# Kernel tuning notes

Measured on AMD Instinct MI355X. Metric: run time of the kernel, lower is better.

Reference implementation:

```python
import jax, jax.numpy as jnp
import numpy as np

EPS = 1e-6
CHUNK = 128  # chunk size for the causal linear-attention scan


def elu_plus_one(x):
    return jax.nn.elu(x) + 1.0


def causal_linear_attention(q, k, v):
    # out_t = (sq_t @ cumsum_{j<=t} sk_j v_j^T) / (sq_t . cumsum_{j<=t} sk_j), clamped
    B, S, D = q.shape
    sq = elu_plus_one(q)
    sk = elu_plus_one(k)
    N = S // CHUNK
    # [N, B, C, D] chunked layout for scan over chunks
    sq_c = sq.reshape(B, N, CHUNK, D).transpose(1, 0, 2, 3)
    sk_c = sk.reshape(B, N, CHUNK, D).transpose(1, 0, 2, 3)
    v_c = v.reshape(B, N, CHUNK, D).transpose(1, 0, 2, 3)
    mask = jnp.tril(jnp.ones((CHUNK, CHUNK), dtype=q.dtype))  # inclusive causal

    def step(carry, inp):
        S_kv, z = carry  # [B,D,D], [B,D] running sums from previous chunks
        sqi, ski, vi = inp
        A = jnp.einsum('bid,bjd->bij', sqi, ski) * mask  # intra-chunk causal scores
        num = jnp.einsum('bij,bje->bie', A, vi) + jnp.einsum('bid,bde->bie', sqi, S_kv)
        den = A.sum(-1) + jnp.einsum('bid,bd->bi', sqi, z)
        out = num / jnp.clip(den, EPS, None)[..., None]
        S_kv = S_kv + jnp.einsum('bcd,bce->bde', ski, vi)
        z = z + ski.sum(axis=1)
        return (S_kv, z), out

    init = (jnp.zeros((B, D, D), q.dtype), jnp.zeros((B, D), q.dtype))
    _, outs = jax.lax.scan(step, init, (sq_c, sk_c, v_c))
    return outs.transpose(1, 0, 2, 3).reshape(B, S, D)


def setup_inputs() -> dict:
    key = jax.random.key(0)
    ks = jax.random.split(key, 8)
    B, S, D = 2, 2048, 1024
    scale = 1.0 / np.sqrt(D)  # realistic init scale for the D x D projections
    return {
        'hidden_states': jax.random.normal(ks[0], (B, S, D), jnp.float32),
        'w_q': jax.random.normal(ks[1], (D, D), jnp.float32) * scale,
        'w_k': jax.random.normal(ks[2], (D, D), jnp.float32) * scale,
        'w_v': jax.random.normal(ks[3], (D, D), jnp.float32) * scale,
        'w_o': jax.random.normal(ks[4], (D, D), jnp.float32) * scale,
        'gate': jnp.zeros((1,), jnp.float32),
        'memory': jax.random.uniform(ks[5], (D, D), jnp.float32) * 0.01,
        'memory_norm': jax.random.uniform(ks[6], (D,), jnp.float32),
    }


def reference(hidden_states, w_q, w_k, w_v, w_o, gate, memory, memory_norm):
    # Projections (torch Linear: x @ W^T)
    q = hidden_states @ w_q.T
    k = hidden_states @ w_k.T
    v = hidden_states @ w_v.T

    # Retrieve from compressive memory (single bank)
    sigma_q = elu_plus_one(q)
    a_mem = sigma_q @ memory
    norm = jnp.clip(sigma_q @ memory_norm, EPS, None)[..., None]
    active = (memory_norm.sum() >= EPS).astype(q.dtype)
    memory_output = active * (a_mem / norm)

    local_output = causal_linear_attention(q, k, v)

    g = jax.nn.sigmoid(gate)  # [1], broadcasts
    output = g * memory_output + (1.0 - g) * local_output
    return output @ w_o.T
```

## Files before the change

kernel.cpp:

```cpp
#include <hip/hip_runtime.h>
#include <cstddef>

#define EPSF 1e-6f

constexpr int D   = 1024;
constexpr int Bv  = 2;
constexpr int S   = 2048;
constexpr int M   = Bv * S;
constexpr int CH  = 256;
constexpr int NCH = S / CH;

constexpr int TSZ  = 128 * 32;
constexpr int TA64 = 64 * 32;

typedef __attribute__((ext_vector_type(8))) short short8;
typedef __attribute__((ext_vector_type(4))) float floatx4;

__device__ __forceinline__ float elu1(float x) { return x > 0.f ? x + 1.f : __expf(x); }
__device__ __forceinline__ float sigmoidf_(float x) { return 1.f / (1.f + __expf(-x)); }
__device__ __forceinline__ unsigned short f2bf(float x) {
    unsigned u = __float_as_uint(x);
    return (unsigned short)((u + 0x7fffu + ((u >> 16) & 1u)) >> 16);
}
__device__ __forceinline__ float bf2f(unsigned short h) {
    return __uint_as_float(((unsigned)h) << 16);
}
__device__ __forceinline__ float wave_reduce(float x) {
#pragma unroll
    for (int off = 32; off > 0; off >>= 1) x += __shfl_down(x, off);
    return x;
}

__device__ __forceinline__ void gl_lds16(const unsigned short* g, unsigned short* l) {
    __builtin_amdgcn_global_load_lds(
        (const __attribute__((address_space(1))) void*)g,
        (__attribute__((address_space(3))) void*)l, 16, 0, 0);
}

__device__ __forceinline__ void gemm256_8ph(const unsigned short* __restrict__ Ag,
                                            const unsigned short* __restrict__ Bg,
                                            unsigned short* sm, int tid,
                                            floatx4 acc[8][4]) {
    const int lane = tid & 63, w = tid >> 6;
    const int wr = w >> 2, wc = w & 3;
    const int fr = lane & 15, gq = lane >> 4;
    const int swz = fr & 7;

    const int r0 = tid >> 3;
    const int c0 = (tid & 7) ^ (r0 & 7);
    const int r1 = (tid + 512) >> 3;
    const int c1 = ((tid + 512) & 7) ^ (r1 & 7);
    const size_t so0 = (size_t)r0 * D + (size_t)c0 * 8;
    const size_t so1 = (size_t)r1 * D + (size_t)c1 * 8;
    unsigned short* const dst0 = sm + tid * 8;
    unsigned short* const dst1 = sm + (tid + 512) * 8;

    auto STG = [&](int kt, int b, int which) {
        const unsigned short* Gs = ((which) < 2 ? Ag : Bg)
            + (size_t)(((which) & 1) * 128) * D + (size_t)(kt) * 64;
        const int slot = (((b) << 2) + (which)) << 13;
        gl_lds16(Gs + so0, dst0 + slot);
        gl_lds16(Gs + so1, dst1 + slot);
    };

    STG(0, 0, 0); STG(0, 0, 1); STG(0, 0, 2); STG(0, 0, 3);
    STG(1, 1, 2); STG(1, 1, 3);
    asm volatile("s_waitcnt vmcnt(4)" ::: "memory");
    __builtin_amdgcn_s_barrier();

    const int NT = D / 64;
    for (int u = 0; u < NT; ++u) {
        const int bu = u & 1;
        const unsigned short* Ah = sm + (((bu << 2) + wr) << 13);
        const unsigned short* Bh = sm + (((bu << 2) + 2 + (wc >> 1)) << 13);
        const int brow = (wc & 1) * 64;
        short8 bfr[4][2];
#pragma unroll
        for (int s = 0; s < 4; ++s) {
            short8 afr[2][2];
#pragma unroll
            for (int i2 = 0; i2 < 2; ++i2)
#pragma unroll
                for (int ks = 0; ks < 2; ++ks)
                    afr[i2][ks] = *(const short8*)&Ah[((s * 2 + i2) * 16 + fr) * 64
                                                      + ((((ks << 2) + gq) ^ swz) << 3)];
            if (s == 0) {
#pragma unroll
                for (int j = 0; j < 4; ++j)
#pragma unroll
                    for (int ks = 0; ks < 2; ++ks)
                        bfr[j][ks] = *(const short8*)&Bh[(brow + j * 16 + fr) * 64
                                                         + ((((ks << 2) + gq) ^ swz) << 3)];
            }
            if (s == 0)      { if (u + 1 < NT) STG(u + 1, bu ^ 1, 0); }
            else if (s == 1) { if (u + 1 < NT) STG(u + 1, bu ^ 1, 1); }
            else if (s == 2) { if (u + 2 < NT) STG(u + 2, bu, 2); }
            else {
                if (u + 2 < NT) {
                    STG(u + 2, bu, 3);
                    asm volatile("s_waitcnt vmcnt(4)" ::: "memory");
                } else if (u + 1 < NT) {
                    asm volatile("s_waitcnt vmcnt(0)" ::: "memory");
                }
            }
            __builtin_amdgcn_s_barrier();
            __builtin_amdgcn_s_setprio(1);
#pragma unroll
            for (int i2 = 0; i2 < 2; ++i2)
#pragma unroll
                for (int j = 0; j < 4; ++j)
#pragma unroll
                    for (int ks = 0; ks < 2; ++ks)
                        acc[s * 2 + i2][j] = __builtin_amdgcn_mfma_f32_16x16x32_bf16(
                            afr[i2][ks], bfr[j][ks], acc[s * 2 + i2][j], 0, 0, 0);
            __builtin_amdgcn_s_setprio(0);
            __builtin_amdgcn_s_barrier();
        }
    }
}

__device__ __forceinline__ void stage128x32(const unsigned short* g, int stride,
                                            unsigned short* lds, int wave, int lane) {
    const int t   = (wave << 6) + lane;
    const int row = t >> 2;
    const int cb  = (((t & 3) ^ ((row >> 1) & 3)) << 3);
    unsigned short* l0 = lds + (wave << 9);
    gl_lds16(g + (size_t)row * stride + cb, l0);
    gl_lds16(g + (size_t)(row + 64) * stride + cb, l0 + 2048);
}

__device__ __forceinline__ void stage64x32(const unsigned short* g, int stride,
                                           unsigned short* lds, int wave, int lane) {
    const int t   = (wave << 6) + lane;
    const int row = t >> 2;
    const int cb  = (((t & 3) ^ ((row >> 1) & 3)) << 3);
    gl_lds16(g + (size_t)row * stride + cb, lds + (wave << 9));
}

__device__ __forceinline__ void mfma_step(const unsigned short* As, const unsigned short* Bs,
                                          int wm, int wn, int fr, int g, floatx4 acc[4][4]) {
    const int off = ((g ^ ((fr >> 1) & 3)) << 3);
    short8 af[4], bf[4];
#pragma unroll
    for (int i = 0; i < 4; ++i) af[i] = *(const short8*)&As[(wm + i * 16 + fr) * 32 + off];
#pragma unroll
    for (int j = 0; j < 4; ++j) bf[j] = *(const short8*)&Bs[(wn + j * 16 + fr) * 32 + off];
#pragma unroll
    for (int i = 0; i < 4; ++i)
#pragma unroll
        for (int j = 0; j < 4; ++j)
            acc[i][j] = __builtin_amdgcn_mfma_f32_16x16x32_bf16(af[i], bf[j], acc[i][j], 0, 0, 0);
}

__device__ __forceinline__ void mfma_step64d(const unsigned short* As, const unsigned short* Bs,
                                             int wm, int wn, int fr, int g,
                                             floatx4 acc[2][4], floatx4 accd[2], short8 bones) {
    const int off = ((g ^ ((fr >> 1) & 3)) << 3);
    short8 af[2], bf[4];
#pragma unroll
    for (int i = 0; i < 2; ++i) af[i] = *(const short8*)&As[(wm + i * 16 + fr) * 32 + off];
#pragma unroll
    for (int j = 0; j < 4; ++j) bf[j] = *(const short8*)&Bs[(wn + j * 16 + fr) * 32 + off];
#pragma unroll
    for (int i = 0; i < 2; ++i) {
#pragma unroll
        for (int j = 0; j < 4; ++j)
            acc[i][j] = __builtin_amdgcn_mfma_f32_16x16x32_bf16(af[i], bf[j], acc[i][j], 0, 0, 0);
        accd[i] = __builtin_amdgcn_mfma_f32_16x16x32_bf16(af[i], bones, accd[i], 0, 0, 0);
    }
}

__device__ __forceinline__ void mfma_step64(const unsigned short* As, const unsigned short* Bs,
                                            int wm, int wn, int fr, int g, floatx4 acc[2][4]) {
    const int off = ((g ^ ((fr >> 1) & 3)) << 3);
    short8 af[2], bf[4];
#pragma unroll
    for (int i = 0; i < 2; ++i) af[i] = *(const short8*)&As[(wm + i * 16 + fr) * 32 + off];
#pragma unroll
    for (int j = 0; j < 4; ++j) bf[j] = *(const short8*)&Bs[(wn + j * 16 + fr) * 32 + off];
#pragma unroll
    for (int i = 0; i < 2; ++i)
#pragma unroll
        for (int j = 0; j < 4; ++j)
            acc[i][j] = __builtin_amdgcn_mfma_f32_16x16x32_bf16(af[i], bf[j], acc[i][j], 0, 0, 0);
}

__device__ __forceinline__ void gemm_loop_db(const unsigned short* Ag, int strideA,
                                             const unsigned short* Bg, int strideB, int Kk,
                                             unsigned short* As, unsigned short* Bs,
                                             int wave, int lane, int wm, int wn, int fr, int g,
                                             floatx4 acc[4][4]) {
    __syncthreads();
    stage128x32(Ag, strideA, As, wave, lane);
    stage128x32(Bg, strideB, Bs, wave, lane);
    int buf = 0;
    for (int k0 = 32; k0 < Kk; k0 += 32) {
        __syncthreads();
        const int nb = buf ^ 1;
        stage128x32(Ag + k0, strideA, As + nb * TSZ, wave, lane);
        stage128x32(Bg + k0, strideB, Bs + nb * TSZ, wave, lane);
        mfma_step(As + buf * TSZ, Bs + buf * TSZ, wm, wn, fr, g, acc);
        buf = nb;
    }
    __syncthreads();
    mfma_step(As + buf * TSZ, Bs + buf * TSZ, wm, wn, fr, g, acc);
}

__device__ __forceinline__ void gemm_loop_db64d(const unsigned short* Ag, int strideA,
                                                const unsigned short* Bg, int strideB, int Kk,
                                                unsigned short* As, unsigned short* Bs,
                                                int wave, int lane, int wm, int wn, int fr, int g,
                                                floatx4 acc[2][4], floatx4 accd[2], short8 bones) {
    __syncthreads();
    stage64x32(Ag, strideA, As, wave, lane);
    stage128x32(Bg, strideB, Bs, wave, lane);
    int buf = 0;
    for (int k0 = 32; k0 < Kk; k0 += 32) {
        __syncthreads();
        const int nb = buf ^ 1;
        stage64x32(Ag + k0, strideA, As + nb * TA64, wave, lane);
        stage128x32(Bg + k0, strideB, Bs + nb * TSZ, wave, lane);
        mfma_step64d(As + buf * TA64, Bs + buf * TSZ, wm, wn, fr, g, acc, accd, bones);
        buf = nb;
    }
    __syncthreads();
    mfma_step64d(As + buf * TA64, Bs + buf * TSZ, wm, wn, fr, g, acc, accd, bones);
}

__device__ __forceinline__ void gemm_loop_db64(const unsigned short* Ag, int strideA,
                                               const unsigned short* Bg, int strideB, int Kk,
                                               unsigned short* As, unsigned short* Bs,
                                               int wave, int lane, int wm, int wn, int fr, int g,
                                               floatx4 acc[2][4]) {
    __syncthreads();
    stage64x32(Ag, strideA, As, wave, lane);
    stage128x32(Bg, strideB, Bs, wave, lane);
    int buf = 0;
    for (int k0 = 32; k0 < Kk; k0 += 32) {
        __syncthreads();
        const int nb = buf ^ 1;
        stage64x32(Ag + k0, strideA, As + nb * TA64, wave, lane);
        stage128x32(Bg + k0, strideB, Bs + nb * TSZ, wave, lane);
        mfma_step64(As + buf * TA64, Bs + buf * TSZ, wm, wn, fr, g, acc);
        buf = nb;
    }
    __syncthreads();
    mfma_step64(As + buf * TA64, Bs + buf * TSZ, wm, wn, fr, g, acc);
}

__global__ __launch_bounds__(256) void prep(const float* __restrict__ h,
                                            const float* __restrict__ w_q, const float* __restrict__ w_k,
                                            const float* __restrict__ w_v, const float* __restrict__ w_o,
                                            const float* __restrict__ memory,
                                            unsigned short* __restrict__ h_b,
                                            unsigned short* __restrict__ wq_b, unsigned short* __restrict__ wk_b,
                                            unsigned short* __restrict__ wv_b, unsigned short* __restrict__ wo_b,
                                            unsigned short* __restrict__ memT)
{
    __shared__ unsigned short T[64][72];
    const int id = blockIdx.x, tid = threadIdx.x;
    if (id < 4096) {
        const size_t i = ((size_t)id * 256 + tid) * 4;
        float4 v = *(const float4*)(h + i);
        ushort4 o; o.x = f2bf(v.x); o.y = f2bf(v.y); o.z = f2bf(v.z); o.w = f2bf(v.w);
        *(ushort4*)(h_b + i) = o;
    } else if (id < 8192) {
        const int t = id - 4096, which = t >> 10;
        const float* in = (which == 0) ? w_q : (which == 1) ? w_k : (which == 2) ? w_v : w_o;
        unsigned short* out = (which == 0) ? wq_b : (which == 1) ? wk_b : (which == 2) ? wv_b : wo_b;
        const size_t i = ((size_t)(t & 1023) * 256 + tid) * 4;
        float4 v = *(const float4*)(in + i);
        ushort4 o; o.x = f2bf(v.x); o.y = f2bf(v.y); o.z = f2bf(v.z); o.w = f2bf(v.w);
        *(ushort4*)(out + i) = o;
    } else {
        const int t = id - 8192;
        const int d0 = (t >> 4) * 64, e0 = (t & 15) * 64;
        const int r = tid >> 4, c4 = (tid & 15) * 4;
        for (int rr = r; rr < 64; rr += 16) {
            float4 v = *(const float4*)(memory + (size_t)(d0 + rr) * D + e0 + c4);
            T[rr][c4 + 0] = f2bf(v.x); T[rr][c4 + 1] = f2bf(v.y);
            T[rr][c4 + 2] = f2bf(v.z); T[rr][c4 + 3] = f2bf(v.w);
        }
        __syncthreads();
        for (int rr = r; rr < 64; rr += 16) {
            ushort4 o;
            o.x = T[c4 + 0][rr]; o.y = T[c4 + 1][rr];
            o.z = T[c4 + 2][rr]; o.w = T[c4 + 3][rr];
            *(ushort4*)(memT + (size_t)(e0 + rr) * D + d0 + c4) = o;
        }
    }
}

__global__ __launch_bounds__(512, 2) void proj8(const unsigned short* __restrict__ h_b,
                                                const unsigned short* __restrict__ wq,
                                                const unsigned short* __restrict__ wk,
                                                const unsigned short* __restrict__ wv,
                                                unsigned short* __restrict__ sq,
                                                unsigned short* __restrict__ sk,
                                                unsigned short* __restrict__ v)
{
    extern __shared__ unsigned short sm[];
    const int id = blockIdx.x;
    const int x = id & 7, y = id >> 3;
    const int strip = x + 8 * (y % 6);
    const int nn = y / 6;
    const int sub = strip >> 4, m = strip & 15;
    const int m0 = m * 256, n0 = nn * 256;
    const unsigned short* Ag = h_b + (size_t)m0 * D;
    const unsigned short* Bg = ((sub == 0) ? wq : (sub == 1) ? wk : wv) + (size_t)n0 * D;
    unsigned short* C = (sub == 0) ? sq : (sub == 1) ? sk : v;

    const int tid = threadIdx.x;
    const int w = tid >> 6, lane = tid & 63;
    const int wr = w >> 2, wc = w & 3;
    const int fr = lane & 15, gq = lane >> 4;

    floatx4 acc[8][4] = {};
    gemm256_8ph(Ag, Bg, sm, tid, acc);

    const int q4 = gq * 4;
#pragma unroll
    for (int i = 0; i < 8; ++i)
#pragma unroll
        for (int j = 0; j < 4; ++j) {
            const int col = n0 + wc * 64 + j * 16 + fr;
#pragma unroll
            for (int r = 0; r < 4; ++r) {
                const int row = m0 + wr * 128 + i * 16 + q4 + r;
                float val = acc[i][j][r];
                if (sub < 2) val = elu1(val);
                C[(size_t)row * D + col] = f2bf(val);
            }
        }
}

__global__ __launch_bounds__(512, 2) void stage2n(const unsigned short* __restrict__ sq,
                                                  const unsigned short* __restrict__ sk,
                                                  const unsigned short* __restrict__ memT,
                                                  const unsigned short* __restrict__ v_b,
                                                  const float* __restrict__ mnorm,
                                                  const float* __restrict__ gate,
                                                  unsigned short* __restrict__ combm,
                                                  unsigned short* __restrict__ Sbuf2,
                                                  unsigned short* __restrict__ vT,
                                                  float* __restrict__ rowscale)
{
    extern __shared__ unsigned short sm[];
    const int id = blockIdx.x, tid = threadIdx.x;

    if (id < 136) {
        const int wk = (id & 7) * 17 + (id >> 3);
        const int w = tid >> 6, lane = tid & 63;
        const int wr = w >> 2, wc = w & 3;
        const int fr = lane & 15, gq = lane >> 4;
        const int q4 = gq * 4;

        if (wk < 64) {
            const int mt = wk >> 2, nt = wk & 3;
            const int m0 = mt * 256, n0 = nt * 256;
            floatx4 acc[8][4] = {};
            gemm256_8ph(sq + (size_t)m0 * D, memT + (size_t)n0 * D, sm, tid, acc);
#pragma unroll
            for (int i = 0; i < 8; ++i)
#pragma unroll
                for (int j = 0; j < 4; ++j) {
                    const int col = n0 + wc * 64 + j * 16 + fr;
#pragma unroll
                    for (int r = 0; r < 4; ++r)
                        combm[(size_t)(m0 + wr * 128 + i * 16 + q4 + r) * D + col]
                            = f2bf(acc[i][j][r]);
                }
        } else {
            const int w2 = wk - 64;
            const int b = w2 / 36, p = w2 % 36;
            int c = 0;
            while ((c + 1) * (c + 2) / 2 <= p) ++c;
            const int jc = p - c * (c + 1) / 2;
            floatx4 acc[8][4] = {};
            gemm256_8ph(sq + ((size_t)b * S + (size_t)c * CH) * D,
                        sk + ((size_t)b * S + (size_t)jc * CH) * D, sm, tid, acc);
            unsigned short* Srow0 = Sbuf2 + (size_t)(b * NCH + c) * CH * S + jc * CH;
            const bool diag = (jc == c);
#pragma unroll
            for (int i = 0; i < 8; ++i)
#pragma unroll
                for (int j = 0; j < 4; ++j) {
                    const int col = wc * 64 + j * 16 + fr;
#pragma unroll
                    for (int r = 0; r < 4; ++r) {
                        const int row = wr * 128 + i * 16 + q4 + r;
                        float val = acc[i][j][r];
                        if (diag && col > row) val = 0.f;
                        Srow0[(size_t)row * S + col] = f2bf(val);
                    }
                }
        }
    } else if (id < 136 + 1024) {
        unsigned short (*T)[72] = (unsigned short(*)[72])sm;
        const int t = id - 136;
        const int b = t >> 9, rem = t & 511;
        const int s0 = (rem >> 4) * 64, d0 = (rem & 15) * 64;
        const int r = tid >> 4, c4 = (tid & 15) * 4;
        const unsigned short* ip = v_b + (size_t)b * S * D;
        for (int rr = r; rr < 64; rr += 32) {
            ushort4 vv = *(const ushort4*)(ip + (size_t)(s0 + rr) * D + d0 + c4);
            T[rr][c4 + 0] = vv.x; T[rr][c4 + 1] = vv.y; T[rr][c4 + 2] = vv.z; T[rr][c4 + 3] = vv.w;
        }
        __syncthreads();
        unsigned short* op = vT + (size_t)b * D * S;
        for (int rr = r; rr < 64; rr += 32) {
            ushort4 o;
            o.x = T[c4 + 0][rr]; o.y = T[c4 + 1][rr];
            o.z = T[c4 + 2][rr]; o.w = T[c4 + 3][rr];
            *(ushort4*)(op + (size_t)(d0 + rr) * S + s0 + c4) = o;
        }
    } else {
        const int wave = tid >> 6, lane = tid & 63;
        const int row = (id - 136 - 1024) * 8 + wave;
        const unsigned short* sr = sq + (size_t)row * D;
        float dot = 0.f, msum = 0.f;
#pragma unroll
        for (int p = 0; p < 2; ++p) {
            const int d0 = p * 512 + lane * 8;
            short8 sv = *(const short8*)(sr + d0);
            float4 m0 = *(const float4*)(mnorm + d0);
            float4 m1 = *(const float4*)(mnorm + d0 + 4);
            dot += bf2f((unsigned short)sv[0]) * m0.x + bf2f((unsigned short)sv[1]) * m0.y
                 + bf2f((unsigned short)sv[2]) * m0.z + bf2f((unsigned short)sv[3]) * m0.w
                 + bf2f((unsigned short)sv[4]) * m1.x + bf2f((unsigned short)sv[5]) * m1.y
                 + bf2f((unsigned short)sv[6]) * m1.z + bf2f((unsigned short)sv[7]) * m1.w;
            msum += m0.x + m0.y + m0.z + m0.w + m1.x + m1.y + m1.z + m1.w;
        }
        dot = wave_reduce(dot);
        msum = wave_reduce(msum);
        if (lane == 0) {
            const float gg = sigmoidf_(gate[0]);
            const float active = (msum >= EPSF) ? 1.f : 0.f;
            rowscale[row] = gg * active / fmaxf(dot, EPSF);
        }
    }
}

__global__ __launch_bounds__(256) void proj_fused(const unsigned short* __restrict__ h_b,
                                                  const unsigned short* __restrict__ wq,
                                                  const unsigned short* __restrict__ wk,
                                                  const unsigned short* __restrict__ wv,
                                                  unsigned short* __restrict__ sq,
                                                  unsigned short* __restrict__ sk,
                                                  unsigned short* __restrict__ v)
{
    __shared__ unsigned short As[2 * TSZ], Bs[2 * TSZ];
    const int id = blockIdx.x;
    const int x = id & 7, y = id >> 3;
    const int strip = x + 8 * (y % 12);
    const int n     = y / 12;
    const int sub = strip >> 5, m = strip & 31;
    const int m0 = m * 128, n0 = n * 128;
    const unsigned short* B = (sub == 0) ? wq : (sub == 1) ? wk : wv;
    unsigned short* C = (sub == 0) ? sq : (sub == 1) ? sk : v;

    const int tid = threadIdx.x, wave = tid >> 6, lane = tid & 63;
    const int wm = (wave >> 1) * 64, wn = (wave & 1) * 64;
    const int fr = lane & 15, g = lane >> 4;
    const int q4 = g * 4;

    floatx4 acc[4][4] = {};
    gemm_loop_db(h_b + (size_t)m0 * D, D, B + (size_t)n0 * D, D, D,
                 As, Bs, wave, lane, wm, wn, fr, g, acc);

#pragma unroll
    for (int i = 0; i < 4; ++i)
#pragma unroll
        for (int j = 0; j < 4; ++j) {
            const int col = n0 + wn + j * 16 + fr;
#pragma unroll
            for (int r = 0; r < 4; ++r) {
                const int row = m0 + wm + i * 16 + q4 + r;
                float val = acc[i][j][r];
                if (sub < 2) val = elu1(val);
                C[(size_t)row * D + col] = f2bf(val);
            }
        }
}

__global__ __launch_bounds__(256) void stage2(const unsigned short* __restrict__ sq,
                                              const unsigned short* __restrict__ sk,
                                              const unsigned short* __restrict__ memT,
                                              const unsigned short* __restrict__ v_b,
                                              const float* __restrict__ mnorm,
                                              const float* __restrict__ gate,
                                              unsigned short* __restrict__ combm,
                                              unsigned short* __restrict__ Sbuf2,
                                              unsigned short* __restrict__ vT,
                                              float* __restrict__ rowscale)
{
    __shared__ unsigned short As[2 * TSZ], Bs[2 * TSZ];
    const int id = blockIdx.x, tid = threadIdx.x;
    const int wave = tid >> 6, lane = tid & 63;
    const int wm = (wave >> 1) * 64, wn = (wave & 1) * 64;
    const int fr = lane & 15, g = lane >> 4;
    const int q4 = g * 4;

    if (id < 256) {
        const int x = id & 7, y = id >> 3;
        const int m0 = (x + 8 * (y & 3)) * 128;
        const int n0 = (y >> 2) * 128;
        floatx4 acc[4][4] = {};
        gemm_loop_db(sq + (size_t)m0 * D, D, memT + (size_t)n0 * D, D, D,
                     As, Bs, wave, lane, wm, wn, fr, g, acc);
#pragma unroll
        for (int i = 0; i < 4; ++i)
#pragma unroll
            for (int j = 0; j < 4; ++j) {
                const int col = n0 + wn + j * 16 + fr;
#pragma unroll
                for (int r = 0; r < 4; ++r)
                    combm[(size_t)(m0 + wm + i * 16 + q4 + r) * D + col] = f2bf(acc[i][j][r]);
            }
    } else if (id < 544) {
        const int t = id - 256;
        const int b = t / 144, rem = t % 144;
        const int p = rem >> 2, tt = rem & 3;
        const int it = tt >> 1, jt = tt & 1;
        int c = 0;
        while ((c + 1) * (c + 2) / 2 <= p) ++c;
        const int j = p - c * (c + 1) / 2;
        unsigned short* Srow0 = Sbuf2 + (size_t)(b * NCH + c) * CH * S;

        if (j == c && jt > it) {
            const int row = it * 128 + (tid >> 1);
            unsigned short* zp = Srow0 + (size_t)row * S + j * CH + jt * 128 + (tid & 1) * 64;
            uint4 z4 = make_uint4(0, 0, 0, 0);
#pragma unroll
            for (int i = 0; i < 8; ++i) *(uint4*)(zp + i * 8) = z4;
            return;
        }
        floatx4 acc[4][4] = {};
        gemm_loop_db(sq + ((size_t)b * S + (size_t)c * CH + it * 128) * D, D,
                     sk + ((size_t)b * S + (size_t)j * CH + jt * 128) * D, D, D,
                     As, Bs, wave, lane, wm, wn, fr, g, acc);
        const bool diag = (j == c && it == jt);
#pragma unroll
        for (int i = 0; i < 4; ++i)
#pragma unroll
            for (int jj = 0; jj < 4; ++jj) {
                const int col = jt * 128 + wn + jj * 16 + fr;
#pragma unroll
                for (int r = 0; r < 4; ++r) {
                    const int row = it * 128 + wm + i * 16 + q4 + r;
                    float val = acc[i][jj][r];
                    if (diag && col > row) val = 0.f;
                    Srow0[(size_t)row * S + j * CH + col] = f2bf(val);
                }
            }
    } else if (id < 1568) {
        unsigned short (*T)[72] = (unsigned short(*)[72])As;
        const int t = id - 544;
        const int b = t >> 9, rem = t & 511;
        const int s0 = (rem >> 4) * 64, d0 = (rem & 15) * 64;
        const int r = tid >> 4, c4 = (tid & 15) * 4;
        const unsigned short* ip = v_b + (size_t)b * S * D;
        for (int rr = r; rr < 64; rr += 16) {
            ushort4 vv = *(const ushort4*)(ip + (size_t)(s0 + rr) * D + d0 + c4);
            T[rr][c4 + 0] = vv.x; T[rr][c4 + 1] = vv.y; T[rr][c4 + 2] = vv.z; T[rr][c4 + 3] = vv.w;
        }
        __syncthreads();
        unsigned short* op = vT + (size_t)b * D * S;
        for (int rr = r; rr < 64; rr += 16) {
            ushort4 o;
            o.x = T[c4 + 0][rr]; o.y = T[c4 + 1][rr];
            o.z = T[c4 + 2][rr]; o.w = T[c4 + 3][rr];
            *(ushort4*)(op + (size_t)(d0 + rr) * S + s0 + c4) = o;
        }
    } else {
        const int row = (id - 1568) * 4 + wave;
        const unsigned short* sr = sq + (size_t)row * D;
        float dot = 0.f, msum = 0.f;
#pragma unroll
        for (int p = 0; p < 2; ++p) {
            const int d0 = p * 512 + lane * 8;
            short8 sv = *(const short8*)(sr + d0);
            float4 m0 = *(const float4*)(mnorm + d0);
            float4 m1 = *(const float4*)(mnorm + d0 + 4);
            dot += bf2f((unsigned short)sv[0]) * m0.x + bf2f((unsigned short)sv[1]) * m0.y
                 + bf2f((unsigned short)sv[2]) * m0.z + bf2f((unsigned short)sv[3]) * m0.w
                 + bf2f((unsigned short)sv[4]) * m1.x + bf2f((unsigned short)sv[5]) * m1.y
                 + bf2f((unsigned short)sv[6]) * m1.z + bf2f((unsigned short)sv[7]) * m1.w;
            msum += m0.x + m0.y + m0.z + m0.w + m1.x + m1.y + m1.z + m1.w;
        }
        dot = wave_reduce(dot);
        msum = wave_reduce(msum);
        if (lane == 0) {
            const float gg = sigmoidf_(gate[0]);
            const float active = (msum >= EPSF) ? 1.f : 0.f;
            rowscale[row] = gg * active / fmaxf(dot, EPSF);
        }
    }
}

__global__ __launch_bounds__(256) void pv64(const unsigned short* __restrict__ Sbuf2,
                                            const unsigned short* __restrict__ vT,
                                            const float* __restrict__ rowscale,
                                            const float* __restrict__ gate,
                                            unsigned short* __restrict__ combm)
{
    __shared__ unsigned short As2[2 * TA64], Bs2[2 * TSZ];
    const int id = blockIdx.x, tid = threadIdx.x;
    const int wave = tid >> 6, lane = tid & 63;
    const int wm = (wave >> 1) * 32, wn = (wave & 1) * 64;
    const int fr = lane & 15, g = lane >> 4;
    const int q4 = g * 4;

    const int x = id & 7, y = id >> 3;
    const int g_ = x + 8 * (y & 7);
    const int e  = y >> 3;
    const int b = g_ >> 5;
    const int rem = g_ & 31;
    const int c = (NCH - 1) - (rem >> 2);
    const int i0 = (rem & 3) * 64, e0 = e * 128;

    const short one_bf = (short)0x3F80;
    short8 bones = {one_bf, one_bf, one_bf, one_bf, one_bf, one_bf, one_bf, one_bf};

    floatx4 acc[2][4] = {};
    floatx4 accd[2] = {};
    gemm_loop_db64d(Sbuf2 + ((size_t)(b * NCH + c) * CH + i0) * S, S,
                    vT + (size_t)b * D * S + (size_t)e0 * S, S, (c + 1) * CH,
                    As2, Bs2, wave, lane, wm, wn, fr, g, acc, accd, bones);

    const float gg = sigmoidf_(gate[0]);
    const float wloc = 1.f - gg;
#pragma unroll
    for (int i = 0; i < 2; ++i)
#pragma unroll
        for (int j = 0; j < 4; ++j) {
            const int col = e0 + wn + j * 16 + fr;
#pragma unroll
            for (int r = 0; r < 4; ++r) {
                const int li = i0 + wm + i * 16 + q4 + r;
                const int rg = b * S + c * CH + li;
                const float inv = wloc / fmaxf(accd[i][r], EPSF);
                const size_t idx = (size_t)rg * D + col;
                combm[idx] = f2bf(bf2f(combm[idx]) * rowscale[rg] + acc[i][j][r] * inv);
            }
        }
}

__global__ __launch_bounds__(256) void outproj64(const unsigned short* __restrict__ A,
                                                 const unsigned short* __restrict__ wo,
                                                 float* __restrict__ out)
{
    __shared__ unsigned short As2[2 * TA64], Bs2[2 * TSZ];
    const int id = blockIdx.x, tid = threadIdx.x;
    const int wave = tid >> 6, lane = tid & 63;
    const int wm = (wave >> 1) * 32, wn = (wave & 1) * 64;
    const int fr = lane & 15, g = lane >> 4;
    const int q4 = g * 4;

    const int x = id & 7, y = id >> 3;
    const int m0 = (x + 8 * (y & 7)) * 64;
    const int n0 = (y >> 3) * 128;

    floatx4 acc[2][4] = {};
    gemm_loop_db64(A + (size_t)m0 * D, D, wo + (size_t)n0 * D, D, D,
                   As2, Bs2, wave, lane, wm, wn, fr, g, acc);

#pragma unroll
    for (int i = 0; i < 2; ++i)
#pragma unroll
        for (int j = 0; j < 4; ++j) {
            const int col = n0 + wn + j * 16 + fr;
#pragma unroll
            for (int r = 0; r < 4; ++r)
                out[(size_t)(m0 + wm + i * 16 + q4 + r) * D + col] = acc[i][j][r];
        }
}

extern "C" void kernel_launch(void* const* d_in, const int* in_sizes, int n_in,
                              void* d_out, int out_size, void* d_ws, size_t ws_size,
                              hipStream_t stream)
{
    const float* h      = (const float*)d_in[0];
    const float* w_q    = (const float*)d_in[1];
    const float* w_k    = (const float*)d_in[2];
    const float* w_v    = (const float*)d_in[3];
    const float* w_o    = (const float*)d_in[4];
    const float* gate   = (const float*)d_in[5];
    const float* memory = (const float*)d_in[6];
    const float* mnorm  = (const float*)d_in[7];
    float* out = (float*)d_out;

    unsigned short* h_b   = (unsigned short*)d_ws;
    unsigned short* wq_b  = h_b + (size_t)M * D;
    unsigned short* wk_b  = wq_b + (size_t)D * D;
    unsigned short* wv_b  = wk_b + (size_t)D * D;
    unsigned short* wo_b  = wv_b + (size_t)D * D;
    unsigned short* memT  = wo_b + (size_t)D * D;
    unsigned short* sq_b  = memT + (size_t)D * D;
    unsigned short* sk_b  = sq_b + (size_t)M * D;
    unsigned short* v_b   = sk_b + (size_t)M * D;
    unsigned short* vT    = v_b + (size_t)M * D;
    unsigned short* Sbuf2 = vT + (size_t)M * D;
    unsigned short* combm = Sbuf2 + (size_t)Bv * NCH * CH * S;
    float* rowscale = (float*)(combm + (size_t)M * D);

    dim3 blk(256);

    prep<<<8448, blk, 0, stream>>>(h, w_q, w_k, w_v, w_o, memory,
                                   h_b, wq_b, wk_b, wv_b, wo_b, memT);

    static const bool lds128_ok = [] {
        bool a = hipFuncSetAttribute(reinterpret_cast<const void*>(proj8),
                                     hipFuncAttributeMaxDynamicSharedMemorySize,
                                     131072) == hipSuccess;
        bool b = hipFuncSetAttribute(reinterpret_cast<const void*>(stage2n),
                                     hipFuncAttributeMaxDynamicSharedMemorySize,
                                     131072) == hipSuccess;
        return a && b;
    }();

    if (lds128_ok) {
        proj8<<<192, dim3(512), 131072, stream>>>(h_b, wq_b, wk_b, wv_b, sq_b, sk_b, v_b);
        stage2n<<<1672, dim3(512), 131072, stream>>>(sq_b, sk_b, memT, v_b, mnorm, gate,
                                                     combm, Sbuf2, vT, rowscale);
    } else {
        proj_fused<<<768, blk, 0, stream>>>(h_b, wq_b, wk_b, wv_b, sq_b, sk_b, v_b);
        stage2<<<2592, blk, 0, stream>>>(sq_b, sk_b, memT, v_b, mnorm, gate,
                                         combm, Sbuf2, vT, rowscale);
    }

    pv64<<<512, blk, 0, stream>>>(Sbuf2, vT, rowscale, gate, combm);
    outproj64<<<512, blk, 0, stream>>>(combm, wo_b, out);
}
```

Measured before the change: 218.4 us.

## Retile pv and output-projection GEMMs to 64x64 tiles with K-step 64

Changes the pv64 and outproj64 GEMM tiles from 64x128 with K-step 32 to 64x64 with K-step 64. This uses a new 64x64 LDS staging routine with an XOR swizzle and doubles the grid to 1024 blocks. The aim is more blocks to fill the 256 CUs and half as many barriers per K. The cost is lower arithmetic intensity per block and more redundant loads of the A tiles.

```diff
diff --git a/kernel.cpp b/kernel.cpp
--- a/kernel.cpp
+++ b/kernel.cpp
@@ -12,6 +12,7 @@
 
 constexpr int TSZ  = 128 * 32;
 constexpr int TA64 = 64 * 32;
+constexpr int T66  = 64 * 64;
 
 typedef __attribute__((ext_vector_type(8))) short short8;
 typedef __attribute__((ext_vector_type(4))) float floatx4;
@@ -137,6 +138,18 @@
     gl_lds16(g + (size_t)row * stride + cb, lds + (wave << 9));
 }
 
+__device__ __forceinline__ void stage64x64(const unsigned short* g, int stride,
+                                           unsigned short* lds, int wave, int lane) {
+    const int base = (wave << 6) + lane;
+    const int c8   = (lane & 7) ^ (lane >> 3);
+#pragma unroll
+    for (int q = 0; q < 2; ++q) {
+        const int P   = (q << 8) + base;
+        const int row = P >> 3;
+        gl_lds16(g + (size_t)row * stride + (c8 << 3), lds + (q << 11) + (wave << 9));
+    }
+}
+
 __device__ __forceinline__ void mfma_step(const unsigned short* As, const unsigned short* Bs,
                                           int wm, int wn, int fr, int g, floatx4 acc[4][4]) {
     const int off = ((g ^ ((fr >> 1) & 3)) << 3);
@@ -152,37 +165,45 @@
             acc[i][j] = __builtin_amdgcn_mfma_f32_16x16x32_bf16(af[i], bf[j], acc[i][j], 0, 0, 0);
 }
 
-__device__ __forceinline__ void mfma_step64d(const unsigned short* As, const unsigned short* Bs,
-                                             int wm, int wn, int fr, int g,
-                                             floatx4 acc[2][4], floatx4 accd[2], short8 bones) {
-    const int off = ((g ^ ((fr >> 1) & 3)) << 3);
-    short8 af[2], bf[4];
-#pragma unroll
-    for (int i = 0; i < 2; ++i) af[i] = *(const short8*)&As[(wm + i * 16 + fr) * 32 + off];
-#pragma unroll
-    for (int j = 0; j < 4; ++j) bf[j] = *(const short8*)&Bs[(wn + j * 16 + fr) * 32 + off];
-#pragma unroll
-    for (int i = 0; i < 2; ++i) {
-#pragma unroll
-        for (int j = 0; j < 4; ++j)
-            acc[i][j] = __builtin_amdgcn_mfma_f32_16x16x32_bf16(af[i], bf[j], acc[i][j], 0, 0, 0);
-        accd[i] = __builtin_amdgcn_mfma_f32_16x16x32_bf16(af[i], bones, accd[i], 0, 0, 0);
-    }
-}
-
-__device__ __forceinline__ void mfma_step64(const unsigned short* As, const unsigned short* Bs,
-                                            int wm, int wn, int fr, int g, floatx4 acc[2][4]) {
-    const int off = ((g ^ ((fr >> 1) & 3)) << 3);
-    short8 af[2], bf[4];
-#pragma unroll
-    for (int i = 0; i < 2; ++i) af[i] = *(const short8*)&As[(wm + i * 16 + fr) * 32 + off];
-#pragma unroll
-    for (int j = 0; j < 4; ++j) bf[j] = *(const short8*)&Bs[(wn + j * 16 + fr) * 32 + off];
-#pragma unroll
-    for (int i = 0; i < 2; ++i)
-#pragma unroll
-        for (int j = 0; j < 4; ++j)
-            acc[i][j] = __builtin_amdgcn_mfma_f32_16x16x32_bf16(af[i], bf[j], acc[i][j], 0, 0, 0);
+__device__ __forceinline__ void mfma_6464d(const unsigned short* As, const unsigned short* Bs,
+                                           int wm, int wn, int fr, int g,
+                                           floatx4 acc[2][2], floatx4 accd[2], short8 bones) {
+    const int x7 = fr & 7;
+#pragma unroll
+    for (int s = 0; s < 2; ++s) {
+        const int off = ((g + 4 * s) ^ x7) << 3;
+        short8 af[2], bf[2];
+#pragma unroll
+        for (int i = 0; i < 2; ++i) af[i] = *(const short8*)&As[(wm + i * 16 + fr) * 64 + off];
+#pragma unroll
+        for (int j = 0; j < 2; ++j) bf[j] = *(const short8*)&Bs[(wn + j * 16 + fr) * 64 + off];
+#pragma unroll
+        for (int i = 0; i < 2; ++i) {
+#pragma unroll
+            for (int j = 0; j < 2; ++j)
+                acc[i][j] = __builtin_amdgcn_mfma_f32_16x16x32_bf16(af[i], bf[j], acc[i][j], 0, 0, 0);
+            accd[i] = __builtin_amdgcn_mfma_f32_16x16x32_bf16(af[i], bones, accd[i], 0, 0, 0);
+        }
+    }
+}
+
+__device__ __forceinline__ void mfma_6464(const unsigned short* As, const unsigned short* Bs,
+                                          int wm, int wn, int fr, int g, floatx4 acc[2][2]) {
+    const int x7 = fr & 7;
+#pragma unroll
+    for (int s = 0; s < 2; ++s) {
+        const int off = ((g + 4 * s) ^ x7) << 3;
+        short8 af[2], bf[2];
+#pragma unroll
+        for (int i = 0; i < 2; ++i) af[i] = *(const short8*)&As[(wm + i * 16 + fr) * 64 + off];
+#pragma unroll
+        for (int j = 0; j < 2; ++j) bf[j] = *(const short8*)&Bs[(wn + j * 16 + fr) * 64 + off];
+#pragma unroll
+        for (int i = 0; i < 2; ++i)
+#pragma unroll
+            for (int j = 0; j < 2; ++j)
+                acc[i][j] = __builtin_amdgcn_mfma_f32_16x16x32_bf16(af[i], bf[j], acc[i][j], 0, 0, 0);
+    }
 }
 
 __device__ __forceinline__ void gemm_loop_db(const unsigned short* Ag, int strideA,
@@ -206,46 +227,46 @@
     mfma_step(As + buf * TSZ, Bs + buf * TSZ, wm, wn, fr, g, acc);
 }
 
-__device__ __forceinline__ void gemm_loop_db64d(const unsigned short* Ag, int strideA,
-                                                const unsigned short* Bg, int strideB, int Kk,
+__device__ __forceinline__ void gemm_loop_6464d(const unsigned short* Ag, int sA,
+                                                const unsigned short* Bg, int sB, int Kk,
                                                 unsigned short* As, unsigned short* Bs,
                                                 int wave, int lane, int wm, int wn, int fr, int g,
-                                                floatx4 acc[2][4], floatx4 accd[2], short8 bones) {
+                                                floatx4 acc[2][2], floatx4 accd[2], short8 bones) {
     __syncthreads();
-    stage64x32(Ag, strideA, As, wave, lane);
-    stage128x32(Bg, strideB, Bs, wave, lane);
+    stage64x64(Ag, sA, As, wave, lane);
+    stage64x64(Bg, sB, Bs, wave, lane);
     int buf = 0;
-    for (int k0 = 32; k0 < Kk; k0 += 32) {
+    for (int k0 = 64; k0 < Kk; k0 += 64) {
         __syncthreads();
         const int nb = buf ^ 1;
-        stage64x32(Ag + k0, strideA, As + nb * TA64, wave, lane);
-        stage128x32(Bg + k0, strideB, Bs + nb * TSZ, wave, lane);
-        mfma_step64d(As + buf * TA64, Bs + buf * TSZ, wm, wn, fr, g, acc, accd, bones);
+        stage64x64(Ag + k0, sA, As + nb * T66, wave, lane);
+        stage64x64(Bg + k0, sB, Bs + nb * T66, wave, lane);
+        mfma_6464d(As + buf * T66, Bs + buf * T66, wm, wn, fr, g, acc, accd, bones);
         buf = nb;
     }
     __syncthreads();
-    mfma_step64d(As + buf * TA64, Bs + buf * TSZ, wm, wn, fr, g, acc, accd, bones);
-}
-
-__device__ __forceinline__ void gemm_loop_db64(const unsigned short* Ag, int strideA,
-                                               const unsigned short* Bg, int strideB, int Kk,
+    mfma_6464d(As + buf * T66, Bs + buf * T66, wm, wn, fr, g, acc, accd, bones);
+}
+
+__device__ __forceinline__ void gemm_loop_6464(const unsigned short* Ag, int sA,
+                                               const unsigned short* Bg, int sB, int Kk,
                                                unsigned short* As, unsigned short* Bs,
                                                int wave, int lane, int wm, int wn, int fr, int g,
-                                               floatx4 acc[2][4]) {
+                                               floatx4 acc[2][2]) {
     __syncthreads();
-    stage64x32(Ag, strideA, As, wave, lane);
-    stage128x32(Bg, strideB, Bs, wave, lane);
+    stage64x64(Ag, sA, As, wave, lane);
+    stage64x64(Bg, sB, Bs, wave, lane);
     int buf = 0;
-    for (int k0 = 32; k0 < Kk; k0 += 32) {
+    for (int k0 = 64; k0 < Kk; k0 += 64) {
         __syncthreads();
         const int nb = buf ^ 1;
-        stage64x32(Ag + k0, strideA, As + nb * TA64, wave, lane);
-        stage128x32(Bg + k0, strideB, Bs + nb * TSZ, wave, lane);
-        mfma_step64(As + buf * TA64, Bs + buf * TSZ, wm, wn, fr, g, acc);
+        stage64x64(Ag + k0, sA, As + nb * T66, wave, lane);
+        stage64x64(Bg + k0, sB, Bs + nb * T66, wave, lane);
+        mfma_6464(As + buf * T66, Bs + buf * T66, wm, wn, fr, g, acc);
         buf = nb;
     }
     __syncthreads();
-    mfma_step64(As + buf * TA64, Bs + buf * TSZ, wm, wn, fr, g, acc);
+    mfma_6464(As + buf * T66, Bs + buf * T66, wm, wn, fr, g, acc);
 }
 
 __global__ __launch_bounds__(256) void prep(const float* __restrict__ h,
@@ -604,10 +625,10 @@
                                             const float* __restrict__ gate,
                                             unsigned short* __restrict__ combm)
 {
-    __shared__ unsigned short As2[2 * TA64], Bs2[2 * TSZ];
+    __shared__ unsigned short As2[2 * T66], Bs2[2 * T66];
     const int id = blockIdx.x, tid = threadIdx.x;
     const int wave = tid >> 6, lane = tid & 63;
-    const int wm = (wave >> 1) * 32, wn = (wave & 1) * 64;
+    const int wm = (wave >> 1) * 32, wn = (wave & 1) * 32;
     const int fr = lane & 15, g = lane >> 4;
     const int q4 = g * 4;
 
@@ -617,14 +638,14 @@
     const int b = g_ >> 5;
     const int rem = g_ & 31;
     const int c = (NCH - 1) - (rem >> 2);
-    const int i0 = (rem & 3) * 64, e0 = e * 128;
+    const int i0 = (rem & 3) * 64, e0 = e * 64;
 
     const short one_bf = (short)0x3F80;
     short8 bones = {one_bf, one_bf, one_bf, one_bf, one_bf, one_bf, one_bf, one_bf};
 
-    floatx4 acc[2][4] = {};
+    floatx4 acc[2][2] = {};
     floatx4 accd[2] = {};
-    gemm_loop_db64d(Sbuf2 + ((size_t)(b * NCH + c) * CH + i0) * S, S,
+    gemm_loop_6464d(Sbuf2 + ((size_t)(b * NCH + c) * CH + i0) * S, S,
                     vT + (size_t)b * D * S + (size_t)e0 * S, S, (c + 1) * CH,
                     As2, Bs2, wave, lane, wm, wn, fr, g, acc, accd, bones);
 
@@ -633,7 +654,7 @@
 #pragma unroll
     for (int i = 0; i < 2; ++i)
 #pragma unroll
-        for (int j = 0; j < 4; ++j) {
+        for (int j = 0; j < 2; ++j) {
             const int col = e0 + wn + j * 16 + fr;
 #pragma unroll
             for (int r = 0; r < 4; ++r) {
@@ -650,25 +671,25 @@
                                                  const unsigned short* __restrict__ wo,
                                                  float* __restrict__ out)
 {
-    __shared__ unsigned short As2[2 * TA64], Bs2[2 * TSZ];
+    __shared__ unsigned short As2[2 * T66], Bs2[2 * T66];
     const int id = blockIdx.x, tid = threadIdx.x;
     const int wave = tid >> 6, lane = tid & 63;
-    const int wm = (wave >> 1) * 32, wn = (wave & 1) * 64;
+    const int wm = (wave >> 1) * 32, wn = (wave & 1) * 32;
     const int fr = lane & 15, g = lane >> 4;
     const int q4 = g * 4;
 
     const int x = id & 7, y = id >> 3;
     const int m0 = (x + 8 * (y & 7)) * 64;
-    const int n0 = (y >> 3) * 128;
-
-    floatx4 acc[2][4] = {};
-    gemm_loop_db64(A + (size_t)m0 * D, D, wo + (size_t)n0 * D, D, D,
+    const int n0 = (y >> 3) * 64;
+
+    floatx4 acc[2][2] = {};
+    gemm_loop_6464(A + (size_t)m0 * D, D, wo + (size_t)n0 * D, D, D,
                    As2, Bs2, wave, lane, wm, wn, fr, g, acc);
 
 #pragma unroll
     for (int i = 0; i < 2; ++i)
 #pragma unroll
-        for (int j = 0; j < 4; ++j) {
+        for (int j = 0; j < 2; ++j) {
             const int col = n0 + wn + j * 16 + fr;
 #pragma unroll
             for (int r = 0; r < 4; ++r)
@@ -729,6 +750,6 @@
                                          combm, Sbuf2, vT, rowscale);
     }
 
-    pv64<<<512, blk, 0, stream>>>(Sbuf2, vT, rowscale, gate, combm);
-    outproj64<<<512, blk, 0, stream>>>(combm, wo_b, out);
-}
+    pv64<<<1024, blk, 0, stream>>>(Sbuf2, vT, rowscale, gate, combm);
+    outproj64<<<1024, blk, 0, stream>>>(combm, wo_b, out);
+}
```

Result: faster. 204.2 us (-6.5%).
